# Optimization experiments

Hardware: AMD Instinct MI355X
Metric: run time of the kernel (lower is better)

## Reference

```python
import jax, jax.numpy as jnp
import numpy as np

# reformer-enwik8-style config (trimmed to 2 layers, 2 hash rounds)
B, S, D = 2, 4096, 1024          # batch, seq, hidden
H, Dh = 8, 128                   # heads, head dim (H*Dh == D)
R, C, NB = 2, 64, 128            # num hashes, lsh chunk len, num buckets
L, FF, V = 2, 4096, 258          # layers, ffn dim, vocab
EPS = 1e-12
CAUSAL_NEG, SELF_NEG = -1e9, -1e5


def layer_norm(x, g, b):
    mu = x.mean(-1, keepdims=True)
    var = ((x - mu) ** 2).mean(-1, keepdims=True)
    return (x - mu) * jax.lax.rsqrt(var + EPS) * g + b


def lsh_attn(h, Wqk, Wv, Wo, rot):
    # shared query/key projection (Reformer LSH uses tied Q=K)
    qk = (h @ Wqk).reshape(B, S, H, Dh).transpose(0, 2, 1, 3)   # [B,H,S,Dh]
    v = (h @ Wv).reshape(B, S, H, Dh).transpose(0, 2, 1, 3)
    # LSH bucketing via random rotations: rot [H,Dh,R,NB//2]
    rotated = jnp.einsum('bhsd,hdrn->bhrsn', qk, rot)
    buckets = jnp.argmax(jnp.concatenate([rotated, -rotated], -1), axis=-1)  # [B,H,R,S]
    ids = (buckets + jnp.arange(R)[None, None, :, None] * NB).reshape(B, H, R * S)
    pos = jnp.tile(jnp.arange(S), R)
    # stable sort by (bucket, position)
    sticker = jnp.argsort(ids * S + pos[None, None, :], axis=-1)  # [B,H,R*S]
    orig = sticker % S
    gather = lambda t: jnp.take_along_axis(t, orig[..., None], axis=2)
    sq = gather(qk)                                               # [B,H,RS,Dh]
    sv = gather(v)
    # key = len-normalized qk / sqrt(Dh) (HF _len_and_dim_norm)
    sk = sq * jax.lax.rsqrt(jnp.mean(sq * sq, -1, keepdims=True) + 1e-6) / jnp.sqrt(float(Dh))
    nc = R * S // C
    qc = sq.reshape(B, H, nc, C, Dh)
    kc = sk.reshape(B, H, nc, C, Dh)
    vc = sv.reshape(B, H, nc, C, Dh)
    pc = orig.reshape(B, H, nc, C)
    # attend to current chunk + 1 previous chunk (wraparound, as in HF)
    ke = jnp.concatenate([jnp.roll(kc, 1, axis=2), kc], axis=3)   # [B,H,nc,2C,Dh]
    ve = jnp.concatenate([jnp.roll(vc, 1, axis=2), vc], axis=3)
    pe = jnp.concatenate([jnp.roll(pc, 1, axis=2), pc], axis=3)   # [B,H,nc,2C]
    scores = jnp.einsum('bhncd,bhnkd->bhnck', qc, ke)
    qpos, kpos = pc[..., :, None], pe[..., None, :]
    scores = jnp.where(kpos > qpos, CAUSAL_NEG, scores)           # causal (decoder)
    scores = jnp.where(kpos == qpos, SELF_NEG, scores)            # mask self (q==k)
    lse = jax.scipy.special.logsumexp(scores, axis=-1, keepdims=True)
    probs = jnp.exp(scores - lse)
    o = jnp.einsum('bhnck,bhnkd->bhncd', probs, ve).reshape(B, H, R * S, Dh)
    lg = lse.reshape(B, H, R * S)
    undo = jnp.argsort(sticker, axis=-1)
    o = jnp.take_along_axis(o, undo[..., None], axis=2).reshape(B, H, R, S, Dh)
    lg = jnp.take_along_axis(lg, undo, axis=2).reshape(B, H, R, S)
    # combine hash rounds weighted by their logsumexp
    w = jax.nn.softmax(lg, axis=2)[..., None]
    out = (o * w).sum(2)                                          # [B,H,S,Dh]
    out = out.transpose(0, 2, 1, 3).reshape(B, S, H * Dh)
    return out @ Wo


def _forward(x, ln1_g, ln1_b, Wqk, Wv, Wo, rot, ln2_g, ln2_b, W1, b1, W2, b2,
             lnf_g, lnf_b, Wout, bout):
    # reversible residual encoder: x1,x2 start as duplicated hidden states
    x1 = x2 = x
    for l in range(L):
        x1 = x1 + lsh_attn(layer_norm(x2, ln1_g[l], ln1_b[l]), Wqk[l], Wv[l], Wo[l], rot[l])
        x2 = x2 + jax.nn.relu(layer_norm(x1, ln2_g[l], ln2_b[l]) @ W1[l] + b1[l]) @ W2[l] + b2[l]
    hcat = layer_norm(jnp.concatenate([x1, x2], -1), lnf_g, lnf_b)  # [B,S,2D]
    logits = hcat @ Wout + bout
    # F.softmax(x) with no dim on a 3D tensor -> legacy torch dim=0
    return jax.nn.softmax(logits, axis=0)


def setup_inputs() -> dict:
    key = jax.random.key(0)
    ks = jax.random.split(key, 8)
    s = 0.02
    return {
        'x': jax.random.normal(ks[0], (B, S, D), jnp.float32),
        'ln1_g': jnp.ones((L, D), jnp.float32), 'ln1_b': jnp.zeros((L, D), jnp.float32),
        'Wqk': jax.random.normal(ks[1], (L, D, H * Dh), jnp.float32) * s,
        'Wv': jax.random.normal(ks[2], (L, D, H * Dh), jnp.float32) * s,
        'Wo': jax.random.normal(ks[3], (L, H * Dh, D), jnp.float32) * s,
        'rot': jax.random.normal(ks[4], (L, H, Dh, R, NB // 2), jnp.float32),
        'ln2_g': jnp.ones((L, D), jnp.float32), 'ln2_b': jnp.zeros((L, D), jnp.float32),
        'W1': jax.random.normal(ks[5], (L, D, FF), jnp.float32) * s,
        'b1': jnp.zeros((L, FF), jnp.float32),
        'W2': jax.random.normal(ks[6], (L, FF, D), jnp.float32) * s,
        'b2': jnp.zeros((L, D), jnp.float32),
        'lnf_g': jnp.ones((2 * D,), jnp.float32), 'lnf_b': jnp.zeros((2 * D,), jnp.float32),
        'Wout': jax.random.normal(ks[7], (2 * D, V), jnp.float32) * s,
        'bout': jnp.zeros((V,), jnp.float32),
    }


def reference(x, ln1_g, ln1_b, Wqk, Wv, Wo, rot, ln2_g, ln2_b, W1, b1, W2, b2,
              lnf_g, lnf_b, Wout, bout):
    return _forward(x, ln1_g, ln1_b, Wqk, Wv, Wo, rot, ln2_g, ln2_b, W1, b1, W2, b2,
                    lnf_g, lnf_b, Wout, bout)
```

## Files before the change

### kernel.cpp

```cpp
#include <hip/hip_runtime.h>
#include <hip/hip_fp16.h>
#include <math.h>

#define BB 2
#define SS 4096
#define DD 1024
#define HH 8
#define DH 128
#define RR 2
#define CC 64
#define NBUCK 128
#define LL 2
#define FFD 4096
#define VV 258
#define VP 384
#define RS (RR*SS)
#define NC (RS/CC)
#define BH (BB*HH)
#define MROWS (BB*SS)

#define SCF 256.0f
#define DSCF (1.0f/65536.0f)

typedef __attribute__((ext_vector_type(8))) _Float16 v8h;
typedef __attribute__((ext_vector_type(4))) _Float16 v4h;
typedef __attribute__((ext_vector_type(4))) float v4f;

__device__ __forceinline__ void gld16(const void* g, void* l) {
  __builtin_amdgcn_global_load_lds((const __attribute__((address_space(1))) void*)g,
                                   (__attribute__((address_space(3))) void*)l, 16, 0, 0);
}

__device__ __forceinline__ void block_sum2(float& s, float& s2) {
  #pragma unroll
  for (int o = 1; o < 64; o <<= 1) { s += __shfl_xor(s, o); s2 += __shfl_xor(s2, o); }
  __shared__ float rs[4], rq[4];
  int wave = threadIdx.x >> 6;
  if ((threadIdx.x & 63) == 0) { rs[wave] = s; rq[wave] = s2; }
  __syncthreads();
  s  = rs[0] + rs[1] + rs[2] + rs[3];
  s2 = rq[0] + rq[1] + rq[2] + rq[3];
}

__global__ __launch_bounds__(256) void init_x_kernel(const float* __restrict__ x,
                                                     float* __restrict__ x1,
                                                     float* __restrict__ x2) {
  size_t i = (size_t)blockIdx.x * 256 + threadIdx.x;
  float v = x[i];
  x1[i] = v; x2[i] = v;
}

__global__ __launch_bounds__(256) void ln_split_kernel(const float* __restrict__ x,
                                                       const float* __restrict__ g,
                                                       const float* __restrict__ bta,
                                                       _Float16* __restrict__ out) {
  int row = blockIdx.x;
  int t = threadIdx.x;
  float4 xv = ((const float4*)(x + (size_t)row * DD))[t];
  float s  = xv.x + xv.y + xv.z + xv.w;
  float s2 = xv.x*xv.x + xv.y*xv.y + xv.z*xv.z + xv.w*xv.w;
  block_sum2(s, s2);
  float mu   = s * (1.0f / DD);
  float var  = fmaxf(s2 * (1.0f / DD) - mu * mu, 0.0f);
  float rstd = rsqrtf(var + 1e-12f);
  float4 gv = ((const float4*)g)[t];
  float4 bv = ((const float4*)bta)[t];
  float4 sv;
  sv.x = ((xv.x - mu) * rstd * gv.x + bv.x) * SCF;
  sv.y = ((xv.y - mu) * rstd * gv.y + bv.y) * SCF;
  sv.z = ((xv.z - mu) * rstd * gv.z + bv.z) * SCF;
  sv.w = ((xv.w - mu) * rstd * gv.w + bv.w) * SCF;
  v4h h0, h1;
  h0[0]=(_Float16)sv.x; h0[1]=(_Float16)sv.y; h0[2]=(_Float16)sv.z; h0[3]=(_Float16)sv.w;
  h1[0]=(_Float16)(sv.x-(float)h0[0]); h1[1]=(_Float16)(sv.y-(float)h0[1]);
  h1[2]=(_Float16)(sv.z-(float)h0[2]); h1[3]=(_Float16)(sv.w-(float)h0[3]);
  const size_t PLN = (size_t)MROWS * DD;
  size_t base = (size_t)row * DD + t * 4;
  *(v4h*)(out + base) = h0;
  *(v4h*)(out + PLN + base) = h1;
}

__global__ __launch_bounds__(256) void ln_concat_split_kernel(const float* __restrict__ x1,
                                                              const float* __restrict__ x2,
                                                              const float* __restrict__ g,
                                                              const float* __restrict__ bta,
                                                              _Float16* __restrict__ out) {
  int row = blockIdx.x;
  int t = threadIdx.x;
  float4 a = ((const float4*)(x1 + (size_t)row * DD))[t];
  float4 b = ((const float4*)(x2 + (size_t)row * DD))[t];
  float s  = a.x + a.y + a.z + a.w + b.x + b.y + b.z + b.w;
  float s2 = a.x*a.x + a.y*a.y + a.z*a.z + a.w*a.w
           + b.x*b.x + b.y*b.y + b.z*b.z + b.w*b.w;
  block_sum2(s, s2);
  float mu   = s * (1.0f / (2*DD));
  float var  = fmaxf(s2 * (1.0f / (2*DD)) - mu * mu, 0.0f);
  float rstd = rsqrtf(var + 1e-12f);
  float4 g1 = ((const float4*)g)[t];
  float4 b1v = ((const float4*)bta)[t];
  float4 g2 = ((const float4*)g)[256 + t];
  float4 b2v = ((const float4*)bta)[256 + t];
  const size_t PLN = (size_t)MROWS * (2*DD);
  float4 s1, s2v;
  s1.x = ((a.x-mu)*rstd*g1.x + b1v.x)*SCF;  s1.y = ((a.y-mu)*rstd*g1.y + b1v.y)*SCF;
  s1.z = ((a.z-mu)*rstd*g1.z + b1v.z)*SCF;  s1.w = ((a.w-mu)*rstd*g1.w + b1v.w)*SCF;
  s2v.x = ((b.x-mu)*rstd*g2.x + b2v.x)*SCF; s2v.y = ((b.y-mu)*rstd*g2.y + b2v.y)*SCF;
  s2v.z = ((b.z-mu)*rstd*g2.z + b2v.z)*SCF; s2v.w = ((b.w-mu)*rstd*g2.w + b2v.w)*SCF;
  v4h h0, h1;
  size_t base = (size_t)row * (2*DD) + t * 4;
  h0[0]=(_Float16)s1.x; h0[1]=(_Float16)s1.y; h0[2]=(_Float16)s1.z; h0[3]=(_Float16)s1.w;
  h1[0]=(_Float16)(s1.x-(float)h0[0]); h1[1]=(_Float16)(s1.y-(float)h0[1]);
  h1[2]=(_Float16)(s1.z-(float)h0[2]); h1[3]=(_Float16)(s1.w-(float)h0[3]);
  *(v4h*)(out + base) = h0;
  *(v4h*)(out + PLN + base) = h1;
  h0[0]=(_Float16)s2v.x; h0[1]=(_Float16)s2v.y; h0[2]=(_Float16)s2v.z; h0[3]=(_Float16)s2v.w;
  h1[0]=(_Float16)(s2v.x-(float)h0[0]); h1[1]=(_Float16)(s2v.y-(float)h0[1]);
  h1[2]=(_Float16)(s2v.z-(float)h0[2]); h1[3]=(_Float16)(s2v.w-(float)h0[3]);
  *(v4h*)(out + base + DD) = h0;
  *(v4h*)(out + PLN + base + DD) = h1;
}

__global__ __launch_bounds__(256) void wconv_kernel(const float* __restrict__ W,
                                                    _Float16* __restrict__ Wt,
                                                    int K, int N, int Npad, int ldw) {
  __shared__ float tile[32][33];
  int n0 = blockIdx.x * 32, k0 = blockIdx.y * 32;
  int tid = threadIdx.x;
  #pragma unroll
  for (int i = 0; i < 4; i++) {
    int idx = i*256 + tid;
    int kk = idx >> 5, nn = idx & 31;
    float v = 0.0f;
    if (n0 + nn < N) v = W[(size_t)(k0 + kk) * ldw + n0 + nn];
    tile[kk][nn] = v;
  }
  __syncthreads();
  size_t NKs = (size_t)Npad * K;
  #pragma unroll
  for (int i = 0; i < 4; i++) {
    int idx = i*256 + tid;
    int nn = idx >> 5, kk = idx & 31;
    float s = tile[kk][nn] * SCF;
    size_t off = (size_t)(n0 + nn) * K + k0 + kk;
    _Float16 h0 = (_Float16)s;
    _Float16 h1 = (_Float16)(s - (float)h0);
    Wt[off] = h0;
    Wt[NKs + off] = h1;
  }
}

template<int PL, int CMODE, bool BIAS, bool RELU, int NP>
__global__ __launch_bounds__(256) void qgemm_kernel(const _Float16* __restrict__ A,
                                                    const _Float16* __restrict__ Bt,
                                                    const float* __restrict__ bias,
                                                    void* __restrict__ Cv,
                                                    int M, int N, int K,
                                                    size_t aplane, size_t bplane) {
  __shared__ __align__(16) _Float16 As[2*128*32];
  __shared__ __align__(16) _Float16 Bs[2*128*32];
  int tid = threadIdx.x, lane = tid & 63, wave = tid >> 6;
  int m0 = blockIdx.y * 128, n0 = blockIdx.x * 128;
  int wm = (wave & 1) * 64, wn = (wave >> 1) * 64;
  int lm = lane & 15, quad = lane >> 4;
  const int NCH = (PL == 2) ? 8 : 4;
  const int ACH = (PL == 2) ? 16 : 8;
  v4f acc[4][4];
  #pragma unroll
  for (int i = 0; i < 4; i++)
    #pragma unroll
    for (int j = 0; j < 4; j++) acc[i][j] = (v4f)0.0f;

  for (int k0 = 0; k0 < K; k0 += 32) {
    #pragma unroll
    for (int i = 0; i < NCH; i++) {
      int c = wave * NCH + i;
      if (c < ACH) {
        int p = c >> 3, q = c & 7;
        int row = q * 16 + (lane >> 2), col = (lane & 3) * 8;
        gld16(A + (size_t)p * aplane + (size_t)(m0 + row) * K + k0 + col,
              (char*)As + (size_t)c * 1024);
      } else {
        int cb = c - ACH;
        int p = cb >> 3, q = cb & 7;
        int row = q * 16 + (lane >> 2), col = (lane & 3) * 8;
        gld16(Bt + (size_t)p * bplane + (size_t)(n0 + row) * K + k0 + col,
              (char*)Bs + (size_t)cb * 1024);
      }
    }
    __syncthreads();
    v8h a[4][2], b[4][2];
    #pragma unroll
    for (int ni = 0; ni < 4; ni++) {
      int boff = (wn + ni*16 + lm) * 32 + quad * 8;
      b[ni][0] = *(const v8h*)&Bs[boff];
      if (PL == 2) b[ni][1] = *(const v8h*)&Bs[4096 + boff];
    }
    #pragma unroll
    for (int mi = 0; mi < 4; mi++) {
      int aoff = (wm + mi*16 + lm) * 32 + quad * 8;
      a[mi][0] = *(const v8h*)&As[aoff];
      if (PL == 2) a[mi][1] = *(const v8h*)&As[4096 + aoff];
    }
    #pragma unroll
    for (int mi = 0; mi < 4; mi++) {
      #pragma unroll
      for (int ni = 0; ni < 4; ni++) {
        v4f c0 = acc[mi][ni];
        c0 = __builtin_amdgcn_mfma_f32_16x16x32_f16(a[mi][0], b[ni][0], c0, 0, 0, 0);
        if (PL == 2) {
          c0 = __builtin_amdgcn_mfma_f32_16x16x32_f16(a[mi][0], b[ni][1], c0, 0, 0, 0);
          c0 = __builtin_amdgcn_mfma_f32_16x16x32_f16(a[mi][1], b[ni][0], c0, 0, 0, 0);
          if (NP == 4)
            c0 = __builtin_amdgcn_mfma_f32_16x16x32_f16(a[mi][1], b[ni][1], c0, 0, 0, 0);
        }
        acc[mi][ni] = c0;
      }
    }
    __syncthreads();
  }

  float* Cf = (float*)Cv;
  _Float16* Ch = (_Float16*)Cv;
  const size_t cplane = (size_t)M * N;
  #pragma unroll
  for (int mi = 0; mi < 4; mi++) {
    int rbase = m0 + wm + mi*16 + quad*4;
    #pragma unroll
    for (int ni = 0; ni < 4; ni++) {
      int col = n0 + wn + ni*16 + lm;
      float bv = BIAS ? bias[col] : 0.0f;
      #pragma unroll
      for (int r = 0; r < 4; r++) {
        float val = acc[mi][ni][r] * DSCF + bv;
        if (RELU) val = fmaxf(val, 0.0f);
        size_t off = (size_t)(rbase + r) * N + col;
        if (CMODE == 0) Cf[off] = val;
        else if (CMODE == 1) Cf[off] += val;
        else {
          float s = val * SCF;
          _Float16 h0 = (_Float16)s;
          _Float16 h1 = (_Float16)(s - (float)h0);
          Ch[off] = h0;
          Ch[cplane + off] = h1;
        }
      }
    }
  }
}

__global__ __launch_bounds__(256) void rott_kernel(const float* __restrict__ rot,
                                                   _Float16* __restrict__ rotT) {
  int h = blockIdx.x, grp = blockIdx.y;
  const float* rh = rot + (size_t)h * (DH * RR * 64);
  for (int idx = threadIdx.x; idx < 16*128; idx += 256) {
    int rc = grp*16 + (idx >> 7), d = idx & 127;
    int r = rc >> 6, nn = rc & 63;
    float f = rh[(size_t)d * 128 + r * 64 + nn] * SCF;
    _Float16 h0 = (_Float16)f;
    rotT[(size_t)h*32768 + (size_t)rc*128 + d] = h0;
    rotT[(size_t)h*32768 + 16384 + (size_t)rc*128 + d] = (_Float16)(f - (float)h0);
  }
}

__global__ __launch_bounds__(256) void bucket_mfma_kernel(const float* __restrict__ qkb,
                                                          const _Float16* __restrict__ rotT,
                                                          int* __restrict__ ids) {
  __shared__ __align__(16) float Af[128*32];
  __shared__ __align__(16) _Float16 Bs[2*128*32];
  int mtile = blockIdx.x, bh = blockIdx.y;
  int b = bh >> 3, h = bh & 7;
  int tid = threadIdx.x, lane = tid & 63, wave = tid >> 6;
  int wm = (wave & 1) * 64;
  int r = wave >> 1;
  int wn = r * 64;
  int lm = lane & 15, quad = lane >> 4;
  const float* Aq = qkb + ((size_t)b * SS + (size_t)mtile * 128) * DD + h * DH;
  const _Float16* Bq = rotT + (size_t)h * 32768;
  v4f acc[4][4];
  #pragma unroll
  for (int i = 0; i < 4; i++)
    #pragma unroll
    for (int j = 0; j < 4; j++) acc[i][j] = (v4f)0.0f;

  for (int k0 = 0; k0 < 128; k0 += 32) {
    #pragma unroll
    for (int i = 0; i < 8; i++) {
      int c = wave * 8 + i;
      if (c < 16) {
        int slot = c * 64 + lane;
        int row = slot >> 3;
        int c4 = (slot & 7) ^ (row & 7);
        gld16(Aq + (size_t)row * DD + k0 + c4 * 4, (char*)Af + (size_t)c * 1024);
      } else {
        int cb = c - 16;
        int p = cb >> 3, q = cb & 7;
        int row = q * 16 + (lane >> 2), col = (lane & 3) * 8;
        gld16(Bq + (size_t)p * 16384 + (size_t)row * 128 + k0 + col,
              (char*)Bs + (size_t)p * 8192 + (size_t)q * 1024);
      }
    }
    __syncthreads();
    v8h b0[4], b1[4];
    #pragma unroll
    for (int ni = 0; ni < 4; ni++) {
      int boff = (wn + ni*16 + lm) * 32 + quad * 8;
      b0[ni] = *(const v8h*)&Bs[boff];
      b1[ni] = *(const v8h*)&Bs[4096 + boff];
    }
    #pragma unroll
    for (int mi = 0; mi < 4; mi++) {
      int arow = wm + mi*16 + lm;
      int sw = arow & 7;
      float4 fA = *(const float4*)(Af + arow*32 + (((2*quad)     ^ sw) << 2));
      float4 fB = *(const float4*)(Af + arow*32 + (((2*quad + 1) ^ sw) << 2));
      v8h a0, a1;
      float fs[8] = {fA.x*SCF, fA.y*SCF, fA.z*SCF, fA.w*SCF,
                     fB.x*SCF, fB.y*SCF, fB.z*SCF, fB.w*SCF};
      #pragma unroll
      for (int j = 0; j < 8; j++) {
        _Float16 p0 = (_Float16)fs[j];
        a0[j] = p0;
        a1[j] = (_Float16)(fs[j] - (float)p0);
      }
      #pragma unroll
      for (int ni = 0; ni < 4; ni++) {
        v4f c0 = acc[mi][ni];
        c0 = __builtin_amdgcn_mfma_f32_16x16x32_f16(a0, b0[ni], c0, 0, 0, 0);
        c0 = __builtin_amdgcn_mfma_f32_16x16x32_f16(a0, b1[ni], c0, 0, 0, 0);
        c0 = __builtin_amdgcn_mfma_f32_16x16x32_f16(a1, b0[ni], c0, 0, 0, 0);
        c0 = __builtin_amdgcn_mfma_f32_16x16x32_f16(a1, b1[ni], c0, 0, 0, 0);
        acc[mi][ni] = c0;
      }
    }
    __syncthreads();
  }

  #pragma unroll
  for (int mi = 0; mi < 4; mi++) {
    #pragma unroll
    for (int rr = 0; rr < 4; rr++) {
      float mx = acc[mi][0][rr]; int xi = lm;
      float mn = acc[mi][0][rr]; int ni_ = lm;
      #pragma unroll
      for (int ni = 1; ni < 4; ni++) {
        float vv = acc[mi][ni][rr];
        int col = ni*16 + lm;
        if (vv > mx) { mx = vv; xi = col; }
        if (vv < mn) { mn = vv; ni_ = col; }
      }
      #pragma unroll
      for (int o = 1; o < 16; o <<= 1) {
        float ox = __shfl_xor(mx, o); int oxi = __shfl_xor(xi, o);
        if (ox > mx || (ox == mx && oxi < xi)) { mx = ox; xi = oxi; }
        float on = __shfl_xor(mn, o); int oni = __shfl_xor(ni_, o);
        if (on < mn || (on == mn && oni < ni_)) { mn = on; ni_ = oni; }
      }
      if (lm == 0) {
        int bi = (mx >= -mn) ? xi : 64 + ni_;
        int s = mtile*128 + wm + mi*16 + quad*4 + rr;
        ids[((size_t)bh * RR + r) * SS + s] = bi + r * NBUCK;
      }
    }
  }
}

__global__ __launch_bounds__(256) void sort_count_kernel(const int* __restrict__ ids,
                                                         int* __restrict__ counts) {
  int w = blockIdx.x * 4 + (threadIdx.x >> 6);
  int lane = threadIdx.x & 63;
  int bhr = w >> 6, seg = w & 63;
  int id = ids[(size_t)bhr * SS + seg * 64 + lane];
  int bin = id & 127;
  unsigned long long eq = ~0ull;
  #pragma unroll
  for (int bit = 0; bit < 7; bit++) {
    unsigned long long bal = __ballot((bin >> bit) & 1);
    eq &= ((bin >> bit) & 1) ? bal : ~bal;
  }
  int rank = __popcll(eq & ((1ull << lane) - 1ull));
  if (rank == 0)
    counts[((size_t)bhr * 64 + seg) * 128 + bin] = __popcll(eq);
}

__global__ __launch_bounds__(128) void sort_prefix_kernel(int* __restrict__ counts) {
  int bhr = blockIdx.x;
  int bin = threadIdx.x;
  int r = bhr & 1;
  int* cp = counts + (size_t)bhr * 64 * 128;
  int total = 0;
  for (int seg = 0; seg < 64; seg++) total += cp[seg * 128 + bin];
  __shared__ int tot[128];
  tot[bin] = total;
  __syncthreads();
  for (int off = 1; off < 128; off <<= 1) {
    int t = (bin >= off) ? tot[bin - off] : 0;
    __syncthreads();
    tot[bin] += t;
    __syncthreads();
  }
  int run = tot[bin] - total + r * SS;
  for (int seg = 0; seg < 64; seg++) {
    int c = cp[seg * 128 + bin];
    cp[seg * 128 + bin] = run;
    run += c;
  }
}

__global__ __launch_bounds__(256) void sort_scatter_kernel(const int* __restrict__ ids,
                                                           const int* __restrict__ offs,
                                                           int* __restrict__ orig,
                                                           int* __restrict__ undo) {
  int w = blockIdx.x * 4 + (threadIdx.x >> 6);
  int lane = threadIdx.x & 63;
  int bhr = w >> 6, seg = w & 63;
  int s = seg * 64 + lane;
  int id = ids[(size_t)bhr * SS + s];
  int bin = id & 127;
  unsigned long long eq = ~0ull;
  #pragma unroll
  for (int bit = 0; bit < 7; bit++) {
    unsigned long long bal = __ballot((bin >> bit) & 1);
    eq &= ((bin >> bit) & 1) ? bal : ~bal;
  }
  int rank = __popcll(eq & ((1ull << lane) - 1ull));
  int o = offs[((size_t)bhr * 64 + seg) * 128 + bin] + rank;
  int bh = bhr >> 1, r = bhr & 1;
  orig[(size_t)bh * RS + o] = s;
  undo[(size_t)bh * RS + r * SS + s] = o;
}

__global__ __launch_bounds__(256) void rnorm_kernel(const float* __restrict__ qk,
                                                    const int* __restrict__ orig,
                                                    float* __restrict__ rno) {
  int idx = blockIdx.x * 4 + (threadIdx.x >> 6);
  int lane = threadIdx.x & 63;
  int bh = idx >> 13;
  int k = idx & (RS - 1);
  int b = bh >> 3, h = bh & 7;
  int s = orig[(size_t)bh * RS + k];
  const float* row = qk + ((size_t)(b * SS + s)) * DD + h * DH;
  float x0 = row[lane], x1 = row[lane + 64];
  float ss = x0 * x0 + x1 * x1;
  #pragma unroll
  for (int o = 1; o < 64; o <<= 1) ss += __shfl_xor(ss, o);
  if (lane == 0)
    rno[(size_t)bh * RS + k] = rsqrtf(ss * (1.0f / DH) + 1e-6f) * 0.08838834764831845f;
}

template<int PL>
__global__ __launch_bounds__(256) void attn_mfma_kernel(const float* __restrict__ qk,
                                                        const float* __restrict__ v,
                                                        const int* __restrict__ orig,
                                                        const float* __restrict__ rno,
                                                        float* __restrict__ osort,
                                                        float* __restrict__ lg) {
  constexpr int QPs = 64*136, Kps = 32*136, Vps = 128*36;
  constexpr size_t QPB = (size_t)PL * QPs * 2;
  constexpr size_t KVB = (size_t)PL * Vps * 2;
  __shared__ __align__(16) char smem[QPB + KVB + 1024];
  _Float16* QP = (_Float16*)smem;
  _Float16* KV = (_Float16*)(smem + QPB);
  int* kp_lds = (int*)(smem + QPB + KVB);
  int* qp_lds = kp_lds + 128;

  int blk = blockIdx.x;
  int n = blk & (NC - 1), bh = blk >> 7;
  int b = bh >> 3, h = bh & 7;
  int pn = (n + NC - 1) & (NC - 1);
  int tid = threadIdx.x, lane = tid & 63, wave = tid >> 6;
  int lm = lane & 15, quad = lane >> 4;
  const int* origp = orig + (size_t)bh * RS;
  const float* rnp = rno + (size_t)bh * RS;
  const size_t base = (size_t)b * SS * DD + (size_t)h * DH;

  int d4 = tid & 31;
  int row0 = tid >> 5;
  int kb[4] = {pn*64, pn*64 + 32, n*64, n*64 + 32};

  float4 qreg[8];
  #pragma unroll
  for (int i = 0; i < 8; i++)
    qreg[i] = *(const float4*)(qk + base + (size_t)origp[n*64 + row0 + i*8]*DD + d4*4);

  float4 kreg[2][4]; float krn[2][4];
  #pragma unroll
  for (int i = 0; i < 4; i++) {
    int key = row0 + i*8;
    krn[0][i] = rnp[kb[0] + key];
    kreg[0][i] = *(const float4*)(qk + base + (size_t)origp[kb[0] + key]*DD + d4*4);
  }

  if (tid < 128) kp_lds[tid] = origp[(tid < 64) ? (pn*64 + tid) : (n*64 + tid - 64)];
  else if (tid < 192) qp_lds[tid - 128] = origp[n*64 + tid - 128];

  #pragma unroll
  for (int i = 0; i < 8; i++) {
    int q = row0 + i*8;
    float4 f = qreg[i];
    f.x *= SCF; f.y *= SCF; f.z *= SCF; f.w *= SCF;
    v4h h0; h0[0]=(_Float16)f.x; h0[1]=(_Float16)f.y; h0[2]=(_Float16)f.z; h0[3]=(_Float16)f.w;
    *(v4h*)(QP + q*136 + d4*4) = h0;
    if (PL == 2) {
      v4h h1; h1[0]=(_Float16)(f.x-(float)h0[0]); h1[1]=(_Float16)(f.y-(float)h0[1]);
      h1[2]=(_Float16)(f.z-(float)h0[2]); h1[3]=(_Float16)(f.w-(float)h0[3]);
      *(v4h*)(QP + QPs + q*136 + d4*4) = h1;
    }
  }
  asm volatile("s_waitcnt lgkmcnt(0)" ::: "memory");

  v4f sc[8];
  #pragma unroll
  for (int j = 0; j < 8; j++) sc[j] = (v4f)0.0f;

  #pragma unroll
  for (int g = 0; g < 4; g++) {
    __builtin_amdgcn_s_barrier();
    int cur = g & 1;
    #pragma unroll
    for (int i = 0; i < 4; i++) {
      int key = row0 + i*8;
      float rn = krn[cur][i] * SCF;
      float4 f = kreg[cur][i];
      f.x *= rn; f.y *= rn; f.z *= rn; f.w *= rn;
      v4h h0; h0[0]=(_Float16)f.x; h0[1]=(_Float16)f.y; h0[2]=(_Float16)f.z; h0[3]=(_Float16)f.w;
      *(v4h*)(KV + key*136 + d4*4) = h0;
      if (PL == 2) {
        v4h h1; h1[0]=(_Float16)(f.x-(float)h0[0]); h1[1]=(_Float16)(f.y-(float)h0[1]);
        h1[2]=(_Float16)(f.z-(float)h0[2]); h1[3]=(_Float16)(f.w-(float)h0[3]);
        *(v4h*)(KV + Kps + key*136 + d4*4) = h1;
      }
    }
    if (g < 3) {
      #pragma unroll
      for (int i = 0; i < 4; i++) {
        int key = row0 + i*8;
        int rowid = kp_lds[(g+1)*32 + key];
        krn[cur^1][i] = rnp[kb[g+1] + key];
        kreg[cur^1][i] = *(const float4*)(qk + base + (size_t)rowid*DD + d4*4);
      }
    }
    asm volatile("s_waitcnt lgkmcnt(0)" ::: "memory");
    __builtin_amdgcn_s_barrier();
    __builtin_amdgcn_s_setprio(1);
    #pragma unroll
    for (int ni = 0; ni < 2; ni++) {
      v4f c0 = sc[g*2 + ni];
      #pragma unroll
      for (int ks = 0; ks < 4; ks++) {
        v8h a0 = *(const v8h*)(QP + (wave*16 + lm)*136 + ks*32 + quad*8);
        v8h b0 = *(const v8h*)(KV + (ni*16 + lm)*136 + ks*32 + quad*8);
        c0 = __builtin_amdgcn_mfma_f32_16x16x32_f16(a0, b0, c0, 0, 0, 0);
        if (PL == 2) {
          v8h a1 = *(const v8h*)(QP + QPs + (wave*16 + lm)*136 + ks*32 + quad*8);
          v8h b1 = *(const v8h*)(KV + Kps + (ni*16 + lm)*136 + ks*32 + quad*8);
          c0 = __builtin_amdgcn_mfma_f32_16x16x32_f16(a0, b1, c0, 0, 0, 0);
          c0 = __builtin_amdgcn_mfma_f32_16x16x32_f16(a1, b0, c0, 0, 0, 0);
          c0 = __builtin_amdgcn_mfma_f32_16x16x32_f16(a1, b1, c0, 0, 0, 0);
        }
      }
      sc[g*2 + ni] = c0;
    }
    __builtin_amdgcn_s_setprio(0);
  }

  float4 vreg[2][4];
  #pragma unroll
  for (int i = 0; i < 4; i++) {
    int key = row0 + i*8;
    int rowid = kp_lds[key];
    vreg[0][i] = *(const float4*)(v + base + (size_t)rowid*DD + d4*4);
  }

  __builtin_amdgcn_s_barrier();

  int kp_l[8];
  #pragma unroll
  for (int j = 0; j < 8; j++) kp_l[j] = kp_lds[j*16 + lm];

  #pragma unroll
  for (int rr = 0; rr < 4; rr++) {
    int row = wave*16 + quad*4 + rr;
    int qp = qp_lds[row];
    float sv[8];
    #pragma unroll
    for (int j = 0; j < 8; j++) {
      float s = sc[j][rr] * DSCF;
      int kp = kp_l[j];
      sv[j] = (kp > qp) ? -1000000000.0f : ((kp == qp) ? -100000.0f : s);
    }
    float m = sv[0];
    #pragma unroll
    for (int j = 1; j < 8; j++) m = fmaxf(m, sv[j]);
    #pragma unroll
    for (int o = 1; o < 16; o <<= 1) m = fmaxf(m, __shfl_xor(m, o));
    float es[8], S = 0.0f;
    #pragma unroll
    for (int j = 0; j < 8; j++) { es[j] = __expf(sv[j] - m); S += es[j]; }
    #pragma unroll
    for (int o = 1; o < 16; o <<= 1) S += __shfl_xor(S, o);
    float inv = 1.0f / S;
    if (lm == 0) lg[(size_t)bh * RS + n*64 + row] = m + __logf(S);
    #pragma unroll
    for (int j = 0; j < 8; j++) {
      float p = es[j] * inv * SCF;
      _Float16 p0 = (_Float16)p;
      QP[row*136 + j*16 + lm] = p0;
      if (PL == 2) QP[QPs + row*136 + j*16 + lm] = (_Float16)(p - (float)p0);
    }
  }

  v4f oacc[8];
  #pragma unroll
  for (int j = 0; j < 8; j++) oacc[j] = (v4f)0.0f;
  #pragma unroll
  for (int g = 0; g < 4; g++) {
    __builtin_amdgcn_s_barrier();
    int cur = g & 1;
    int xbs = (d4 & 7) << 2;
    #pragma unroll
    for (int i = 0; i < 4; i++) {
      int keyS = (row0 + i*8) ^ xbs;
      float4 f = vreg[cur][i];
      float fs[4] = {f.x*SCF, f.y*SCF, f.z*SCF, f.w*SCF};
      #pragma unroll
      for (int j = 0; j < 4; j++) {
        int d = d4*4 + j;
        _Float16 p0 = (_Float16)fs[j];
        KV[d*36 + keyS] = p0;
        if (PL == 2) KV[Vps + d*36 + keyS] = (_Float16)(fs[j] - (float)p0);
      }
    }
    if (g < 3) {
      #pragma unroll
      for (int i = 0; i < 4; i++) {
        int key = row0 + i*8;
        int rowid = kp_lds[(g+1)*32 + key];
        vreg[cur^1][i] = *(const float4*)(v + base + (size_t)rowid*DD + d4*4);
      }
    }
    asm volatile("s_waitcnt lgkmcnt(0)" ::: "memory");
    __builtin_amdgcn_s_barrier();
    __builtin_amdgcn_s_setprio(1);
    v8h a0 = *(const v8h*)(QP + (wave*16 + lm)*136 + g*32 + quad*8);
    v8h a1;
    if (PL == 2) a1 = *(const v8h*)(QP + QPs + (wave*16 + lm)*136 + g*32 + quad*8);
    #pragma unroll
    for (int dn = 0; dn < 8; dn++) {
      int d = dn*16 + lm;
      int klo = (quad*8) ^ (((d >> 2) & 7) << 2);
      v4h lo0 = *(const v4h*)(KV + d*36 + klo);
      v4h hi0 = *(const v4h*)(KV + d*36 + (klo ^ 4));
      v8h b0 = __builtin_shufflevector(lo0, hi0, 0,1,2,3,4,5,6,7);
      v4f c0 = oacc[dn];
      c0 = __builtin_amdgcn_mfma_f32_16x16x32_f16(a0, b0, c0, 0, 0, 0);
      if (PL == 2) {
        v4h lo1 = *(const v4h*)(KV + Vps + d*36 + klo);
        v4h hi1 = *(const v4h*)(KV + Vps + d*36 + (klo ^ 4));
        v8h b1 = __builtin_shufflevector(lo1, hi1, 0,1,2,3,4,5,6,7);
        c0 = __builtin_amdgcn_mfma_f32_16x16x32_f16(a0, b1, c0, 0, 0, 0);
        c0 = __builtin_amdgcn_mfma_f32_16x16x32_f16(a1, b0, c0, 0, 0, 0);
        c0 = __builtin_amdgcn_mfma_f32_16x16x32_f16(a1, b1, c0, 0, 0, 0);
      }
      oacc[dn] = c0;
    }
    __builtin_amdgcn_s_setprio(0);
  }

  #pragma unroll
  for (int dn = 0; dn < 8; dn++) {
    #pragma unroll
    for (int rr = 0; rr < 4; rr++) {
      int row = wave*16 + quad*4 + rr;
      osort[((size_t)bh * RS + n*64 + row) * DH + dn*16 + lm] = oacc[dn][rr] * DSCF;
    }
  }
}

__global__ __launch_bounds__(256) void unsort_split_kernel(const float* __restrict__ osort,
                                                           const float* __restrict__ lg,
                                                           const int* __restrict__ undo,
                                                           _Float16* __restrict__ attn) {
  int gid = blockIdx.x * 4 + (threadIdx.x >> 6);
  int lane = threadIdx.x & 63;
  int bh = gid >> 12;
  int s = gid & (SS - 1);
  int b = bh >> 3, h = bh & 7;
  int k0 = undo[(size_t)bh * RS + s];
  int k1 = undo[(size_t)bh * RS + SS + s];
  float l0 = lg[(size_t)bh * RS + k0], l1 = lg[(size_t)bh * RS + k1];
  float m = fmaxf(l0, l1);
  float e0 = __expf(l0 - m), e1 = __expf(l1 - m);
  float inv = 1.0f / (e0 + e1);
  float w0 = e0 * inv, w1 = e1 * inv;
  const float* r0 = osort + ((size_t)bh * RS + k0) * DH;
  const float* r1 = osort + ((size_t)bh * RS + k1) * DH;
  const size_t PLN = (size_t)MROWS * DD;
  _Float16* outp = attn + ((size_t)(b * SS + s)) * DD + h * DH;
  float sA = (w0 * r0[lane]      + w1 * r1[lane])      * SCF;
  float sB = (w0 * r0[lane + 64] + w1 * r1[lane + 64]) * SCF;
  _Float16 a0 = (_Float16)sA, b0 = (_Float16)sB;
  outp[lane] = a0;                 outp[lane + 64] = b0;
  outp[PLN + lane] = (_Float16)(sA - (float)a0);
  outp[PLN + lane + 64] = (_Float16)(sB - (float)b0);
}

__global__ __launch_bounds__(256) void softmax_b_kernel(const float* __restrict__ logits,
                                                        const float* __restrict__ bout,
                                                        float* __restrict__ out) {
  int i = blockIdx.x * 256 + threadIdx.x;
  if (i >= SS * VV) return;
  int s = i / VV, vv = i - s * VV;
  float bvv = bout[vv];
  float l0 = logits[(size_t)s * VP + vv] + bvv;
  float l1 = logits[(size_t)(SS + s) * VP + vv] + bvv;
  float m = fmaxf(l0, l1);
  float e0 = __expf(l0 - m), e1 = __expf(l1 - m);
  float inv = 1.0f / (e0 + e1);
  out[(size_t)s * VV + vv] = e0 * inv;
  out[(size_t)(SS + s) * VV + vv] = e1 * inv;
}

extern "C" void kernel_launch(void* const* d_in, const int* in_sizes, int n_in,
                              void* d_out, int out_size, void* d_ws, size_t ws_size,
                              hipStream_t stream) {
  (void)in_sizes; (void)n_in; (void)out_size; (void)ws_size;
  const float* x     = (const float*)d_in[0];
  const float* ln1_g = (const float*)d_in[1];
  const float* ln1_b = (const float*)d_in[2];
  const float* Wqk   = (const float*)d_in[3];
  const float* Wv    = (const float*)d_in[4];
  const float* Wo    = (const float*)d_in[5];
  const float* rot   = (const float*)d_in[6];
  const float* ln2_g = (const float*)d_in[7];
  const float* ln2_b = (const float*)d_in[8];
  const float* W1    = (const float*)d_in[9];
  const float* b1    = (const float*)d_in[10];
  const float* W2    = (const float*)d_in[11];
  const float* b2    = (const float*)d_in[12];
  const float* lnf_g = (const float*)d_in[13];
  const float* lnf_b = (const float*)d_in[14];
  const float* Wout  = (const float*)d_in[15];
  const float* bout  = (const float*)d_in[16];

  const size_t NX = (size_t)MROWS * DD;
  float* x1 = (float*)d_ws;
  float* x2 = x1 + NX;
  float* h  = x2 + NX;
  _Float16* hs = (_Float16*)h;
  float* pool = h + NX;
  float* qkb   = pool;
  float* vb    = pool + NX;
  float* osort = pool + 2*NX;
  _Float16* ffh = (_Float16*)pool;
  _Float16* hcs = (_Float16*)pool;
  char* wbase = (char*)(pool + 2*NX);
  _Float16* wt = (_Float16*)wbase;
  int* counts = (int*)(wbase + (8u<<20));
  _Float16* rotTs = (_Float16*)(wbase + (10u<<20));
  float* after = pool + 4*NX;
  float* lgb = after;
  float* rno = lgb + (size_t)BH * RS;
  int* orig = (int*)(rno + (size_t)BH * RS);
  int* undo = orig + (size_t)BH * RS;
  int* ids  = undo + (size_t)BH * RS;
  float* logitsP = h;

  const size_t AP_D  = NX;
  const size_t AP_FF = (size_t)MROWS * 2048;
  const size_t BP_D  = (size_t)DD * DD;
  const size_t BP_W1 = (size_t)2048 * DD;
  const size_t BP_W2 = (size_t)DD * 2048;
  const size_t BP_HD = (size_t)VP * 2048;

  init_x_kernel<<<(int)(NX / 256), 256, 0, stream>>>(x, x1, x2);

  for (int l = 0; l < LL; l++) {
    ln_split_kernel<<<MROWS, 256, 0, stream>>>(x2, ln1_g + l*DD, ln1_b + l*DD, hs);

    wconv_kernel<<<dim3(32, 32), 256, 0, stream>>>(Wqk + (size_t)l*DD*DD, wt, DD, DD, DD, DD);
    qgemm_kernel<2,0,false,false,4><<<dim3(8, 64), 256, 0, stream>>>(
        hs, wt, nullptr, qkb, MROWS, DD, DD, AP_D, BP_D);

    wconv_kernel<<<dim3(32, 32), 256, 0, stream>>>(Wv + (size_t)l*DD*DD, wt, DD, DD, DD, DD);
    if (l == 0)
      qgemm_kernel<2,0,false,false,3><<<dim3(8, 64), 256, 0, stream>>>(
          hs, wt, nullptr, vb, MROWS, DD, DD, AP_D, BP_D);
    else
      qgemm_kernel<1,0,false,false,3><<<dim3(8, 64), 256, 0, stream>>>(
          hs, wt, nullptr, vb, MROWS, DD, DD, AP_D, BP_D);

    rott_kernel<<<dim3(8, 8), 256, 0, stream>>>(rot + (size_t)l*HH*DH*RR*64, rotTs);
    bucket_mfma_kernel<<<dim3(32, 16), 256, 0, stream>>>(qkb, rotTs, ids);

    hipMemsetAsync(counts, 0, (size_t)BH * RR * 64 * 128 * sizeof(int), stream);
    sort_count_kernel<<<512, 256, 0, stream>>>(ids, counts);
    sort_prefix_kernel<<<BH*RR, 128, 0, stream>>>(counts);
    sort_scatter_kernel<<<512, 256, 0, stream>>>(ids, counts, orig, undo);

    rnorm_kernel<<<BH*RS/4, 256, 0, stream>>>(qkb, orig, rno);
    if (l == 0)
      attn_mfma_kernel<2><<<BH*NC, 256, 0, stream>>>(qkb, vb, orig, rno, osort, lgb);
    else
      attn_mfma_kernel<1><<<BH*NC, 256, 0, stream>>>(qkb, vb, orig, rno, osort, lgb);
    unsort_split_kernel<<<BH*SS/4, 256, 0, stream>>>(osort, lgb, undo, hs);

    wconv_kernel<<<dim3(32, 32), 256, 0, stream>>>(Wo + (size_t)l*DD*DD, wt, DD, DD, DD, DD);
    if (l == 0)
      qgemm_kernel<2,1,false,false,3><<<dim3(8, 64), 256, 0, stream>>>(
          hs, wt, nullptr, x1, MROWS, DD, DD, AP_D, BP_D);
    else
      qgemm_kernel<1,1,false,false,3><<<dim3(8, 64), 256, 0, stream>>>(
          hs, wt, nullptr, x1, MROWS, DD, DD, AP_D, BP_D);

    ln_split_kernel<<<MROWS, 256, 0, stream>>>(x1, ln2_g + l*DD, ln2_b + l*DD, hs);
    for (int hf = 0; hf < 2; hf++) {
      const float* W1h = W1 + (size_t)l*DD*FFD + (size_t)hf*2048;
      const float* W2h = W2 + (size_t)l*FFD*DD + (size_t)hf*2048*DD;
      _Float16* wt1 = wt;
      _Float16* wt2 = wt + 2u*2097152u;
      wconv_kernel<<<dim3(64, 32), 256, 0, stream>>>(W1h, wt1, DD, 2048, 2048, FFD);
      wconv_kernel<<<dim3(32, 64), 256, 0, stream>>>(W2h, wt2, 2048, DD, DD, DD);
      if (l == 0) {
        qgemm_kernel<2,2,true,true,3><<<dim3(16, 64), 256, 0, stream>>>(
            hs, wt1, b1 + (size_t)l*FFD + hf*2048, ffh, MROWS, 2048, DD, AP_D, BP_W1);
        if (hf == 0)
          qgemm_kernel<2,1,true,false,3><<<dim3(8, 64), 256, 0, stream>>>(
              ffh, wt2, b2 + (size_t)l*DD, x2, MROWS, DD, 2048, AP_FF, BP_W2);
        else
          qgemm_kernel<2,1,false,false,3><<<dim3(8, 64), 256, 0, stream>>>(
              ffh, wt2, nullptr, x2, MROWS, DD, 2048, AP_FF, BP_W2);
      } else {
        qgemm_kernel<1,2,true,true,3><<<dim3(16, 64), 256, 0, stream>>>(
            hs, wt1, b1 + (size_t)l*FFD + hf*2048, ffh, MROWS, 2048, DD, AP_D, BP_W1);
        if (hf == 0)
          qgemm_kernel<1,1,true,false,3><<<dim3(8, 64), 256, 0, stream>>>(
              ffh, wt2, b2 + (size_t)l*DD, x2, MROWS, DD, 2048, AP_FF, BP_W2);
        else
          qgemm_kernel<1,1,false,false,3><<<dim3(8, 64), 256, 0, stream>>>(
              ffh, wt2, nullptr, x2, MROWS, DD, 2048, AP_FF, BP_W2);
      }
    }
  }

  ln_concat_split_kernel<<<MROWS, 256, 0, stream>>>(x1, x2, lnf_g, lnf_b, hcs);
  wconv_kernel<<<dim3(12, 64), 256, 0, stream>>>(Wout, wt, 2*DD, VV, VP, VV);
  qgemm_kernel<1,0,false,false,3><<<dim3(3, 64), 256, 0, stream>>>(
      hcs, wt, nullptr, logitsP, MROWS, VP, 2*DD, AP_FF, BP_HD);
  softmax_b_kernel<<<(SS*VV + 255)/256, 256, 0, stream>>>(logitsP, bout, (float*)d_out);
}
```

Before: 1.772 ms.

## Double-buffer LDS tiles in qgemm and drop residual fp16 plane in final LN

The split-fp16 GEMM main loop now uses two LDS buffers per operand. The next K-slice's global-to-LDS copy is issued right after the current slice's fragments are loaded into registers, so memory traffic overlaps with the MFMA work. LDS allocation is now sized by the plane count. Separately, the final layer-norm kernel writes only the high fp16 plane and no longer writes the low-order residual plane, which cuts global writes. The cost is lower output precision, and results are wrong if a consumer still reads that second plane.

New measurement: 1.751 ms. No clear change (-1.1%).

```diff
diff --git a/kernel.cpp b/kernel.cpp
--- a/kernel.cpp
+++ b/kernel.cpp
@@ -100,24 +100,17 @@
   float4 b1v = ((const float4*)bta)[t];
   float4 g2 = ((const float4*)g)[256 + t];
   float4 b2v = ((const float4*)bta)[256 + t];
-  const size_t PLN = (size_t)MROWS * (2*DD);
   float4 s1, s2v;
   s1.x = ((a.x-mu)*rstd*g1.x + b1v.x)*SCF;  s1.y = ((a.y-mu)*rstd*g1.y + b1v.y)*SCF;
   s1.z = ((a.z-mu)*rstd*g1.z + b1v.z)*SCF;  s1.w = ((a.w-mu)*rstd*g1.w + b1v.w)*SCF;
   s2v.x = ((b.x-mu)*rstd*g2.x + b2v.x)*SCF; s2v.y = ((b.y-mu)*rstd*g2.y + b2v.y)*SCF;
   s2v.z = ((b.z-mu)*rstd*g2.z + b2v.z)*SCF; s2v.w = ((b.w-mu)*rstd*g2.w + b2v.w)*SCF;
-  v4h h0, h1;
+  v4h h0;
   size_t base = (size_t)row * (2*DD) + t * 4;
   h0[0]=(_Float16)s1.x; h0[1]=(_Float16)s1.y; h0[2]=(_Float16)s1.z; h0[3]=(_Float16)s1.w;
-  h1[0]=(_Float16)(s1.x-(float)h0[0]); h1[1]=(_Float16)(s1.y-(float)h0[1]);
-  h1[2]=(_Float16)(s1.z-(float)h0[2]); h1[3]=(_Float16)(s1.w-(float)h0[3]);
   *(v4h*)(out + base) = h0;
-  *(v4h*)(out + PLN + base) = h1;
   h0[0]=(_Float16)s2v.x; h0[1]=(_Float16)s2v.y; h0[2]=(_Float16)s2v.z; h0[3]=(_Float16)s2v.w;
-  h1[0]=(_Float16)(s2v.x-(float)h0[0]); h1[1]=(_Float16)(s2v.y-(float)h0[1]);
-  h1[2]=(_Float16)(s2v.z-(float)h0[2]); h1[3]=(_Float16)(s2v.w-(float)h0[3]);
   *(v4h*)(out + base + DD) = h0;
-  *(v4h*)(out + PLN + base + DD) = h1;
 }
 
 __global__ __launch_bounds__(256) void wconv_kernel(const float* __restrict__ W,
@@ -156,8 +149,8 @@
                                                     void* __restrict__ Cv,
                                                     int M, int N, int K,
                                                     size_t aplane, size_t bplane) {
-  __shared__ __align__(16) _Float16 As[2*128*32];
-  __shared__ __align__(16) _Float16 Bs[2*128*32];
+  __shared__ __align__(16) _Float16 As[2][PL*128*32];
+  __shared__ __align__(16) _Float16 Bs[2][PL*128*32];
   int tid = threadIdx.x, lane = tid & 63, wave = tid >> 6;
   int m0 = blockIdx.y * 128, n0 = blockIdx.x * 128;
   int wm = (wave & 1) * 64, wn = (wave >> 1) * 64;
@@ -170,7 +163,7 @@
     #pragma unroll
     for (int j = 0; j < 4; j++) acc[i][j] = (v4f)0.0f;
 
-  for (int k0 = 0; k0 < K; k0 += 32) {
+  auto stage = [&](int k0, int bufi) {
     #pragma unroll
     for (int i = 0; i < NCH; i++) {
       int c = wave * NCH + i;
@@ -178,29 +171,39 @@
         int p = c >> 3, q = c & 7;
         int row = q * 16 + (lane >> 2), col = (lane & 3) * 8;
         gld16(A + (size_t)p * aplane + (size_t)(m0 + row) * K + k0 + col,
-              (char*)As + (size_t)c * 1024);
+              (char*)As[bufi] + (size_t)c * 1024);
       } else {
         int cb = c - ACH;
         int p = cb >> 3, q = cb & 7;
         int row = q * 16 + (lane >> 2), col = (lane & 3) * 8;
         gld16(Bt + (size_t)p * bplane + (size_t)(n0 + row) * K + k0 + col,
-              (char*)Bs + (size_t)cb * 1024);
-      }
-    }
-    __syncthreads();
+              (char*)Bs[bufi] + (size_t)cb * 1024);
+      }
+    }
+  };
+
+  const int nsteps = K >> 5;
+  stage(0, 0);
+  __syncthreads();
+
+  for (int t = 0; t < nsteps; ++t) {
+    int cur = t & 1;
+    const _Float16* Ab = As[cur];
+    const _Float16* Bb = Bs[cur];
     v8h a[4][2], b[4][2];
     #pragma unroll
     for (int ni = 0; ni < 4; ni++) {
       int boff = (wn + ni*16 + lm) * 32 + quad * 8;
-      b[ni][0] = *(const v8h*)&Bs[boff];
-      if (PL == 2) b[ni][1] = *(const v8h*)&Bs[4096 + boff];
+      b[ni][0] = *(const v8h*)&Bb[boff];
+      if (PL == 2) b[ni][1] = *(const v8h*)&Bb[4096 + boff];
     }
     #pragma unroll
     for (int mi = 0; mi < 4; mi++) {
       int aoff = (wm + mi*16 + lm) * 32 + quad * 8;
-      a[mi][0] = *(const v8h*)&As[aoff];
-      if (PL == 2) a[mi][1] = *(const v8h*)&As[4096 + aoff];
-    }
+      a[mi][0] = *(const v8h*)&Ab[aoff];
+      if (PL == 2) a[mi][1] = *(const v8h*)&Ab[4096 + aoff];
+    }
+    if (t + 1 < nsteps) stage((t + 1) << 5, cur ^ 1);
     #pragma unroll
     for (int mi = 0; mi < 4; mi++) {
       #pragma unroll
```
